# Kernel optimization log

Measured on AMD Instinct MI355X. Metric: run time of the kernel, lower is better.

The kernel has to match this reference:

```python
import jax, jax.numpy as jnp
import numpy as np
import math


def setup_inputs() -> dict:
    key = jax.random.key(0)
    k1, k2, k3 = jax.random.split(key, 3)
    b, h, s, d = 2, 16, 2048, 64
    q = jax.random.normal(k1, (b, h, s, d), dtype=jnp.float32)
    k = jax.random.normal(k2, (b, h, d, s), dtype=jnp.float32)  # pre-transposed as in the torch module
    v = jax.random.normal(k3, (b, h, s, d), dtype=jnp.float32)
    return {"q": q, "k": k, "v": v}


def reference(q, k, v):
    d = q.shape[-1]
    # unnormalized exp-attention, no max subtraction (faithful to source)
    p = jnp.exp(jnp.einsum('bhsd,bhdt->bhst', q, k) / math.sqrt(d))  # [b,h,s,s]
    attn = jnp.einsum('bhst,bhtd->bhsd', p, v)                        # [b,h,s,d]
    l = jnp.sum(p, axis=3, keepdims=True)                             # [b,h,s,1]
    return attn / l
```

## Files before the change

### kernel.cpp

```cpp
#include <hip/hip_runtime.h>

#define S_LEN 2048
#define D_DIM 64
#define BH 32
#define NN ((size_t)BH * S_LEN * D_DIM)

typedef short bf16x8 __attribute__((ext_vector_type(8)));
typedef float f32x16 __attribute__((ext_vector_type(16)));
typedef unsigned int u32x4 __attribute__((ext_vector_type(4)));

static __device__ __forceinline__ unsigned short f2bf(float x) {
  unsigned int u = __float_as_uint(x);
  u += 0x7fffu + ((u >> 16) & 1u);
  return (unsigned short)(u >> 16);
}
static __device__ __forceinline__ float bf2f(unsigned short h) {
  return __uint_as_float(((unsigned int)h) << 16);
}
static __device__ __forceinline__ void gll16(const void* g, void* l) {
  __builtin_amdgcn_global_load_lds((const __attribute__((address_space(1))) void*)g,
                                   (__attribute__((address_space(3))) void*)l, 16, 0, 0);
}

template <bool PERM>
__global__ void transpose_split(const float* __restrict__ in,
                                unsigned short* __restrict__ outh,
                                unsigned short* __restrict__ outl,
                                int R, int C) {
  __shared__ float tile[64][65];
  const int bh = blockIdx.y;
  const int tilesPerRow = C >> 6;
  const int tr = blockIdx.x / tilesPerRow;
  const int tc = blockIdx.x % tilesPerRow;
  const int tid = threadIdx.x;
  const float* src = in + (size_t)bh * R * C;
  {
    const int c4 = (tid & 15) * 4;
    const int r0 = tid >> 4;
#pragma unroll
    for (int rep = 0; rep < 4; ++rep) {
      int r = r0 + rep * 16;
      float4 x = *(const float4*)&src[(size_t)(tr * 64 + r) * C + tc * 64 + c4];
      tile[r][c4] = x.x; tile[r][c4 + 1] = x.y; tile[r][c4 + 2] = x.z; tile[r][c4 + 3] = x.w;
    }
  }
  __syncthreads();
  unsigned short* oh = outh + (size_t)bh * R * C;
  unsigned short* ol = outl + (size_t)bh * R * C;
#pragma unroll
  for (int rep = 0; rep < 2; ++rep) {
    int ci = rep * 256 + tid;
    int orow = ci >> 3;
    int oslot = ci & 7;
    alignas(16) unsigned short hbuf[8];
    alignas(16) unsigned short lbuf[8];
#pragma unroll
    for (int i = 0; i < 8; ++i) {
      int p = oslot * 8 + i;
      int ridx = PERM ? ((p & ~15) | (p & 3) | ((p & 4) << 1) | ((p & 8) >> 1)) : p;
      float x = tile[ridx][orow];
      unsigned short hb = f2bf(x);
      hbuf[i] = hb;
      lbuf[i] = f2bf(x - bf2f(hb));
    }
    size_t o = (size_t)(tc * 64 + orow) * R + tr * 64 + oslot * 8;
    *(int4*)&oh[o] = *(const int4*)hbuf;
    *(int4*)&ol[o] = *(const int4*)lbuf;
  }
}

__global__ __launch_bounds__(256, 2) void attn_fused(
    const float* __restrict__ q, const unsigned short* __restrict__ Khg,
    const unsigned short* __restrict__ Klg, const unsigned short* __restrict__ Vhg,
    const unsigned short* __restrict__ Vlg, float* __restrict__ out) {
  __shared__ __align__(16) unsigned short smem[2][4][64][64];
  __shared__ float Lrow[4][32];

  const int bid = blockIdx.x;
  const int swz = (bid & 7) * 64 + (bid >> 3);
  const int bh = swz >> 4;
  const int qt = swz & 15;
  const int tid = threadIdx.x;
  const int w = tid >> 6;
  const int lane = tid & 63;
  const int l31 = lane & 31;
  const int h = lane >> 5;
  const int q0 = qt * 128 + w * 32;

  bf16x8 qh[4], ql[4];
  {
    const float* qb = q + ((size_t)bh * S_LEN + q0 + l31) * D_DIM;
#pragma unroll
    for (int ks = 0; ks < 4; ++ks) {
      const float* p = qb + ks * 16 + h * 8;
      float4 x0 = *(const float4*)p;
      float4 x1 = *(const float4*)(p + 4);
      float xs[8] = {x0.x, x0.y, x0.z, x0.w, x1.x, x1.y, x1.z, x1.w};
      bf16x8 hh, ll;
#pragma unroll
      for (int j = 0; j < 8; ++j) {
        unsigned short hb = f2bf(xs[j]);
        hh[j] = (short)hb;
        ll[j] = (short)f2bf(xs[j] - bf2f(hb));
      }
      qh[ks] = hh; ql[ks] = ll;
    }
  }

  int rowA[2], gsA[2];
#pragma unroll
  for (int r = 0; r < 2; ++r) {
    int c = (r * 4 + w) * 64 + lane;
    rowA[r] = c >> 3;
    gsA[r] = (c & 7) ^ ((c >> 3) & 7);
  }
  const unsigned short* Kh_b = Khg + (size_t)bh * S_LEN * D_DIM;
  const unsigned short* Kl_b = Klg + (size_t)bh * S_LEN * D_DIM;
  const unsigned short* Vh_b = Vhg + (size_t)bh * D_DIM * S_LEN;
  const unsigned short* Vl_b = Vlg + (size_t)bh * D_DIM * S_LEN;

  auto stage = [&](int buf, int bt) {
#pragma unroll
    for (int r = 0; r < 2; ++r) {
      const int row = rowA[r], gs = gsA[r];
      unsigned short* lbase = &smem[buf][0][0][0] + (r * 4 + w) * 512;
      gll16(Kh_b + (size_t)(bt + row) * 64 + gs * 8, lbase);
      gll16(Kl_b + (size_t)(bt + row) * 64 + gs * 8, lbase + 4096);
      gll16(Vh_b + (size_t)row * S_LEN + bt + gs * 8, lbase + 8192);
      gll16(Vl_b + (size_t)row * S_LEN + bt + gs * 8, lbase + 12288);
    }
  };

  f32x16 o[2] = {};
  float lsum = 0.f;
  const int kx = l31 & 7;

  stage(0, 0);
  __syncthreads();

  int cur = 0;
  for (int kt = 0; kt < 32; ++kt) {
    if (kt < 31) stage(cur ^ 1, (kt + 1) * 64);

    bf16x8 pa[4];
#pragma unroll
    for (int kt2 = 0; kt2 < 2; ++kt2) {
      f32x16 acc = {};
      const int krow = kt2 * 32 + l31;
#pragma unroll
      for (int ks = 0; ks < 4; ++ks) {
        const int sl = ((ks * 2 + h) ^ kx) * 8;
        bf16x8 kh = *(const bf16x8*)&smem[cur][0][krow][sl];
        bf16x8 kl = *(const bf16x8*)&smem[cur][1][krow][sl];
        acc = __builtin_amdgcn_mfma_f32_32x32x16_bf16(kh, qh[ks], acc, 0, 0, 0);
        acc = __builtin_amdgcn_mfma_f32_32x32x16_bf16(kh, ql[ks], acc, 0, 0, 0);
        acc = __builtin_amdgcn_mfma_f32_32x32x16_bf16(kl, qh[ks], acc, 0, 0, 0);
      }
      float pr[16];
#pragma unroll
      for (int i = 0; i < 16; ++i) {
        pr[i] = exp2f(acc[i] * 0.18033688011112042f);
        lsum += pr[i];
      }
#pragma unroll
      for (int s2 = 0; s2 < 2; ++s2) {
        u32x4 wds;
#pragma unroll
        for (int p2 = 0; p2 < 4; ++p2) {
          wds[p2] = (unsigned int)f2bf(pr[s2 * 8 + p2 * 2]) |
                    ((unsigned int)f2bf(pr[s2 * 8 + p2 * 2 + 1]) << 16);
        }
        pa[kt2 * 2 + s2] = __builtin_bit_cast(bf16x8, wds);
      }
    }

#pragma unroll
    for (int s = 0; s < 4; ++s) {
#pragma unroll
      for (int db = 0; db < 2; ++db) {
        const int vrow = db * 32 + l31;
        const int sl = ((s * 2 + h) ^ kx) * 8;
        bf16x8 vh = *(const bf16x8*)&smem[cur][2][vrow][sl];
        bf16x8 vl = *(const bf16x8*)&smem[cur][3][vrow][sl];
        o[db] = __builtin_amdgcn_mfma_f32_32x32x16_bf16(pa[s], vh, o[db], 0, 0, 0);
        o[db] = __builtin_amdgcn_mfma_f32_32x32x16_bf16(pa[s], vl, o[db], 0, 0, 0);
      }
    }

    __syncthreads();
    cur ^= 1;
  }

  float fl = lsum + __shfl_xor(lsum, 32);
  float inv = 1.0f / fl;
  Lrow[w][l31] = inv;
  __syncthreads();
  float linv[16];
#pragma unroll
  for (int r = 0; r < 16; ++r) linv[r] = Lrow[w][(r & 3) + 8 * (r >> 2) + 4 * h];
  float* ob = out + ((size_t)bh * S_LEN + q0) * D_DIM;
#pragma unroll
  for (int db = 0; db < 2; ++db)
#pragma unroll
    for (int r = 0; r < 16; ++r) {
      const int qr = (r & 3) + 8 * (r >> 2) + 4 * h;
      ob[(size_t)qr * D_DIM + db * 32 + l31] = o[db][r] * linv[r];
    }
}

extern "C" void kernel_launch(void* const* d_in, const int* in_sizes, int n_in,
                              void* d_out, int out_size, void* d_ws, size_t ws_size,
                              hipStream_t stream) {
  const float* q = (const float*)d_in[0];
  const float* k = (const float*)d_in[1];
  const float* v = (const float*)d_in[2];
  float* out = (float*)d_out;
  unsigned short* ws = (unsigned short*)d_ws;
  unsigned short* Kh = ws;
  unsigned short* Kl = ws + NN;
  unsigned short* Vh = ws + 2 * NN;
  unsigned short* Vl = ws + 3 * NN;
  transpose_split<false><<<dim3(32, BH), 256, 0, stream>>>(k, Kh, Kl, 64, 2048);
  transpose_split<true><<<dim3(32, BH), 256, 0, stream>>>(v, Vh, Vl, 2048, 64);
  attn_fused<<<dim3(512), 256, 0, stream>>>(q, Kh, Kl, Vh, Vl, out);
}
```

Measured before the change: 190.0 us.

## Drop V low-part split, use packed bf16 convert and MFMA priority hints

Removes the bf16 low-residual component of V, halving the P·V MFMA count and cutting V global loads and LDS staging by one buffer. Replaces the software bf16 rounding of probabilities with the hardware packed convert instruction, and raises wave priority around the MFMA blocks. The trade is lower precision on V, which is now only bf16, and slightly different rounding for P.

```diff
diff --git a/kernel.cpp b/kernel.cpp
--- a/kernel.cpp
+++ b/kernel.cpp
@@ -22,7 +22,7 @@
                                    (__attribute__((address_space(3))) void*)l, 16, 0, 0);
 }
 
-template <bool PERM>
+template <bool PERM, bool LO>
 __global__ void transpose_split(const float* __restrict__ in,
                                 unsigned short* __restrict__ outh,
                                 unsigned short* __restrict__ outl,
@@ -61,19 +61,19 @@
       float x = tile[ridx][orow];
       unsigned short hb = f2bf(x);
       hbuf[i] = hb;
-      lbuf[i] = f2bf(x - bf2f(hb));
+      if (LO) lbuf[i] = f2bf(x - bf2f(hb));
     }
     size_t o = (size_t)(tc * 64 + orow) * R + tr * 64 + oslot * 8;
     *(int4*)&oh[o] = *(const int4*)hbuf;
-    *(int4*)&ol[o] = *(const int4*)lbuf;
+    if (LO) *(int4*)&ol[o] = *(const int4*)lbuf;
   }
 }
 
 __global__ __launch_bounds__(256, 2) void attn_fused(
     const float* __restrict__ q, const unsigned short* __restrict__ Khg,
     const unsigned short* __restrict__ Klg, const unsigned short* __restrict__ Vhg,
-    const unsigned short* __restrict__ Vlg, float* __restrict__ out) {
-  __shared__ __align__(16) unsigned short smem[2][4][64][64];
+    float* __restrict__ out) {
+  __shared__ __align__(16) unsigned short smem[2][3][64][64];
   __shared__ float Lrow[4][32];
 
   const int bid = blockIdx.x;
@@ -117,7 +117,6 @@
   const unsigned short* Kh_b = Khg + (size_t)bh * S_LEN * D_DIM;
   const unsigned short* Kl_b = Klg + (size_t)bh * S_LEN * D_DIM;
   const unsigned short* Vh_b = Vhg + (size_t)bh * D_DIM * S_LEN;
-  const unsigned short* Vl_b = Vlg + (size_t)bh * D_DIM * S_LEN;
 
   auto stage = [&](int buf, int bt) {
 #pragma unroll
@@ -127,7 +126,6 @@
       gll16(Kh_b + (size_t)(bt + row) * 64 + gs * 8, lbase);
       gll16(Kl_b + (size_t)(bt + row) * 64 + gs * 8, lbase + 4096);
       gll16(Vh_b + (size_t)row * S_LEN + bt + gs * 8, lbase + 8192);
-      gll16(Vl_b + (size_t)row * S_LEN + bt + gs * 8, lbase + 12288);
     }
   };
 
@@ -147,6 +145,7 @@
     for (int kt2 = 0; kt2 < 2; ++kt2) {
       f32x16 acc = {};
       const int krow = kt2 * 32 + l31;
+      __builtin_amdgcn_s_setprio(1);
 #pragma unroll
       for (int ks = 0; ks < 4; ++ks) {
         const int sl = ((ks * 2 + h) ^ kx) * 8;
@@ -156,6 +155,7 @@
         acc = __builtin_amdgcn_mfma_f32_32x32x16_bf16(kh, ql[ks], acc, 0, 0, 0);
         acc = __builtin_amdgcn_mfma_f32_32x32x16_bf16(kl, qh[ks], acc, 0, 0, 0);
       }
+      __builtin_amdgcn_s_setprio(0);
       float pr[16];
 #pragma unroll
       for (int i = 0; i < 16; ++i) {
@@ -167,13 +167,17 @@
         u32x4 wds;
 #pragma unroll
         for (int p2 = 0; p2 < 4; ++p2) {
-          wds[p2] = (unsigned int)f2bf(pr[s2 * 8 + p2 * 2]) |
-                    ((unsigned int)f2bf(pr[s2 * 8 + p2 * 2 + 1]) << 16);
+          unsigned int pk;
+          asm("v_cvt_pk_bf16_f32 %0, %1, %2"
+              : "=v"(pk)
+              : "v"(pr[s2 * 8 + p2 * 2]), "v"(pr[s2 * 8 + p2 * 2 + 1]));
+          wds[p2] = pk;
         }
         pa[kt2 * 2 + s2] = __builtin_bit_cast(bf16x8, wds);
       }
     }
 
+    __builtin_amdgcn_s_setprio(1);
 #pragma unroll
     for (int s = 0; s < 4; ++s) {
 #pragma unroll
@@ -181,11 +185,10 @@
         const int vrow = db * 32 + l31;
         const int sl = ((s * 2 + h) ^ kx) * 8;
         bf16x8 vh = *(const bf16x8*)&smem[cur][2][vrow][sl];
-        bf16x8 vl = *(const bf16x8*)&smem[cur][3][vrow][sl];
         o[db] = __builtin_amdgcn_mfma_f32_32x32x16_bf16(pa[s], vh, o[db], 0, 0, 0);
-        o[db] = __builtin_amdgcn_mfma_f32_32x32x16_bf16(pa[s], vl, o[db], 0, 0, 0);
-      }
-    }
+      }
+    }
+    __builtin_amdgcn_s_setprio(0);
 
     __syncthreads();
     cur ^= 1;
@@ -219,8 +222,7 @@
   unsigned short* Kh = ws;
   unsigned short* Kl = ws + NN;
   unsigned short* Vh = ws + 2 * NN;
-  unsigned short* Vl = ws + 3 * NN;
-  transpose_split<false><<<dim3(32, BH), 256, 0, stream>>>(k, Kh, Kl, 64, 2048);
-  transpose_split<true><<<dim3(32, BH), 256, 0, stream>>>(v, Vh, Vl, 2048, 64);
-  attn_fused<<<dim3(512), 256, 0, stream>>>(q, Kh, Kl, Vh, Vl, out);
-}
+  transpose_split<false, true><<<dim3(32, BH), 256, 0, stream>>>(k, Kh, Kl, 64, 2048);
+  transpose_split<true, false><<<dim3(32, BH), 256, 0, stream>>>(v, Vh, nullptr, 2048, 64);
+  attn_fused<<<dim3(512), 256, 0, stream>>>(q, Kh, Kl, Vh, out);
+}
```

Result: faster. 171.6 us (-9.7%).
